# Kernel tuning notes

Hardware: AMD Instinct MI355X
Metric: run time of the kernel (lower is better)

The kernel has to match this reference:

```python
import jax, jax.numpy as jnp
import numpy as np


def _dct_basis_64() -> jnp.ndarray:
    """8x8 2D DCT-II basis as a conv filter of shape [8, 8, 1, 64] (HWIO).

    Filter k = 8*u + v is the (u, v) DCT basis function:
      alpha(u)*alpha(v)*cos((2x+1)u pi/16)*cos((2y+1)v pi/16)
    """
    N = 8
    xs = np.arange(N)
    # 1D DCT matrix: C[u, x]
    C = np.cos((2 * xs[None, :] + 1) * xs[:, None] * np.pi / (2 * N))
    alpha = np.full(N, np.sqrt(2.0 / N))
    alpha[0] = np.sqrt(1.0 / N)
    C = alpha[:, None] * C  # [u, x]
    # basis[x, y, u, v] = C[u, x] * C[v, y]
    basis = np.einsum('ux,vy->xyuv', C, C).reshape(N, N, 1, N * N)
    return jnp.asarray(basis, dtype=jnp.float32)


def setup_inputs() -> dict:
    key = jax.random.key(0)
    inputs = jax.random.normal(key, (16, 256, 256, 1), dtype=jnp.float32)
    dct_basis = _dct_basis_64()  # [8, 8, 1, 64]
    return {"inputs": inputs, "dct_basis": dct_basis}


def reference(inputs, dct_basis):
    # Block DCT: stride-8 SAME conv -> [B, 32, 32, 64]
    x = jax.lax.conv_general_dilated(
        inputs, dct_basis,
        window_strides=(8, 8), padding='SAME',
        dimension_numbers=('NHWC', 'HWIO', 'NHWC'))
    gamma = 1000000.0
    bins = jnp.arange(-60, 61, dtype=x.dtype)  # 121 thresholds
    # Soft CDF at every threshold in one vectorized pass:
    # [B, 121, Hc, Wc, 64] -> sum over spatial -> [B, 121, 64]
    s = jax.nn.sigmoid(gamma * (x[:, None] - bins[None, :, None, None, None]))
    x4 = jnp.sum(s, axis=(2, 3)) / 1024.0
    # Differentiate adjacent soft-CDF values -> 120-bin soft histogram
    x5 = x4[:, 0:120, :] - x4[:, 1:121, :]
    return x5[..., None]  # [B, 120, 64, 1]
```

## Files before the change

### kernel.cpp

```cpp
#include <hip/hip_runtime.h>
#include <math.h>


#define HSTRIDE 121

__global__ __launch_bounds__(64) void dct_hist_kernel(
    const float* __restrict__ in,
    const float* __restrict__ basis,
    float* __restrict__ out)
{
    __shared__ float hist[64 * HSTRIDE];

    const int t  = threadIdx.x;
    const int wg = blockIdx.x;
    const int b  = wg >> 4;
    const int q  = wg & 15;

    #pragma unroll
    for (int i = 0; i < HSTRIDE; ++i) hist[i * 64 + t] = 0.0f;
    __syncthreads();

    float Cm[8][8];
    #pragma unroll
    for (int a = 0; a < 8; ++a)
        #pragma unroll
        for (int x = 0; x < 8; ++x)
            Cm[a][x] = basis[x * 512 + a * 8] * 2.8284271247461903f;

    const int by = q * 2 + (t >> 5);
    const int bx = t & 31;
    const float* p0 = in + ((b * 256 + by * 8) * 256 + bx * 8);

    float tv[8][8];
    #pragma unroll
    for (int x = 0; x < 8; ++x) {
        const float4 r0 = *(const float4*)(p0 + x * 256);
        const float4 r1 = *(const float4*)(p0 + x * 256 + 4);
        const float p[8] = {r0.x, r0.y, r0.z, r0.w, r1.x, r1.y, r1.z, r1.w};
        #pragma unroll
        for (int v = 0; v < 8; ++v) {
            float s = 0.0f;
            #pragma unroll
            for (int y = 0; y < 8; ++y) s = fmaf(Cm[v][y], p[y], s);
            tv[x][v] = s;
        }
    }

    const float EPS = 3e-5f;
    #pragma unroll
    for (int u = 0; u < 8; ++u) {
        #pragma unroll
        for (int v = 0; v < 8; ++v) {
            float xv = 0.0f;
            #pragma unroll
            for (int x = 0; x < 8; ++x) xv = fmaf(Cm[u][x], tv[x][v], xv);
            const int k = u * 8 + v;

            const int j = (int)floorf(xv + 60.0f);
            if (j >= -1 && j <= 120) {
                const float bf  = (float)j - 60.0f;
                const float dlo = xv - bf;
                const float dhi = xv - (bf + 1.0f);
                if (dlo > EPS && dhi < -EPS) {
                    if (j >= 0 && j <= 119) atomicAdd(&hist[k * HSTRIDE + j], 1.0f);
                } else {
                    const float slo = 1.0f / (1.0f + expf(-1e6f * dlo));
                    const float shi = 1.0f / (1.0f + expf(-1e6f * dhi));
                    if (j >= 0 && j <= 119)     atomicAdd(&hist[k * HSTRIDE + j],     slo - shi);
                    if (j - 1 >= 0)             atomicAdd(&hist[k * HSTRIDE + j - 1], 1.0f - slo);
                    if (j + 1 <= 119)           atomicAdd(&hist[k * HSTRIDE + j + 1], shi);
                }
            }
        }
    }

    __syncthreads();

    float* outb = out + b * (120 * 64);
    for (int bin = 0; bin < 120; ++bin) {
        const float v = hist[t * HSTRIDE + bin];
        if (v != 0.0f) atomicAdd(&outb[bin * 64 + t], v * (1.0f / 1024.0f));
    }
}

extern "C" void kernel_launch(void* const* d_in, const int* in_sizes, int n_in,
                              void* d_out, int out_size, void* d_ws, size_t ws_size,
                              hipStream_t stream) {
    const float* inputs = (const float*)d_in[0];
    const float* basis  = (const float*)d_in[1];
    float* out = (float*)d_out;

    (void)hipMemsetAsync(out, 0, (size_t)out_size * sizeof(float), stream);

    dct_hist_kernel<<<dim3(256), dim3(64), 0, stream>>>(inputs, basis, out);
}
```

Before: 72.17 us.

## Use one 1024-thread workgroup per image with privatized LDS histograms

```diff
diff --git a/kernel.cpp b/kernel.cpp
--- a/kernel.cpp
+++ b/kernel.cpp
@@ -3,22 +3,19 @@
 
 
 #define HSTRIDE 121
+#define HCOPY   (64 * HSTRIDE)
 
-__global__ __launch_bounds__(64) void dct_hist_kernel(
+__global__ __launch_bounds__(1024) void dct_hist_kernel(
     const float* __restrict__ in,
     const float* __restrict__ basis,
     float* __restrict__ out)
 {
-    __shared__ float hist[64 * HSTRIDE];
+    __shared__ float hist[2 * HCOPY];
 
-    const int t  = threadIdx.x;
-    const int wg = blockIdx.x;
-    const int b  = wg >> 4;
-    const int q  = wg & 15;
+    const int t = threadIdx.x;
+    const int b = blockIdx.x;
 
-    #pragma unroll
-    for (int i = 0; i < HSTRIDE; ++i) hist[i * 64 + t] = 0.0f;
-    __syncthreads();
+    for (int i = t; i < 2 * HCOPY; i += 1024) hist[i] = 0.0f;
 
     float Cm[8][8];
     #pragma unroll
@@ -27,7 +24,9 @@
         for (int x = 0; x < 8; ++x)
             Cm[a][x] = basis[x * 512 + a * 8] * 2.8284271247461903f;
 
-    const int by = q * 2 + (t >> 5);
+    __syncthreads();
+
+    const int by = t >> 5;
     const int bx = t & 31;
     const float* p0 = in + ((b * 256 + by * 8) * 256 + bx * 8);
 
@@ -46,6 +45,7 @@
         }
     }
 
+    float* h = hist + ((t & 32) ? HCOPY : 0);
     const float EPS = 3e-5f;
     #pragma unroll
     for (int u = 0; u < 8; ++u) {
@@ -62,13 +62,13 @@
                 const float dlo = xv - bf;
                 const float dhi = xv - (bf + 1.0f);
                 if (dlo > EPS && dhi < -EPS) {
-                    if (j >= 0 && j <= 119) atomicAdd(&hist[k * HSTRIDE + j], 1.0f);
+                    if (j >= 0 && j <= 119) atomicAdd(&h[k * HSTRIDE + j], 1.0f);
                 } else {
                     const float slo = 1.0f / (1.0f + expf(-1e6f * dlo));
                     const float shi = 1.0f / (1.0f + expf(-1e6f * dhi));
-                    if (j >= 0 && j <= 119)     atomicAdd(&hist[k * HSTRIDE + j],     slo - shi);
-                    if (j - 1 >= 0)             atomicAdd(&hist[k * HSTRIDE + j - 1], 1.0f - slo);
-                    if (j + 1 <= 119)           atomicAdd(&hist[k * HSTRIDE + j + 1], shi);
+                    if (j >= 0 && j <= 119)     atomicAdd(&h[k * HSTRIDE + j],     slo - shi);
+                    if (j - 1 >= 0)             atomicAdd(&h[k * HSTRIDE + j - 1], 1.0f - slo);
+                    if (j + 1 <= 119)           atomicAdd(&h[k * HSTRIDE + j + 1], shi);
                 }
             }
         }
@@ -77,9 +77,11 @@
     __syncthreads();
 
     float* outb = out + b * (120 * 64);
-    for (int bin = 0; bin < 120; ++bin) {
-        const float v = hist[t * HSTRIDE + bin];
-        if (v != 0.0f) atomicAdd(&outb[bin * 64 + t], v * (1.0f / 1024.0f));
+    for (int idx = t; idx < 120 * 64; idx += 1024) {
+        const int bin = idx >> 6;
+        const int k   = idx & 63;
+        outb[idx] = (hist[k * HSTRIDE + bin] + hist[HCOPY + k * HSTRIDE + bin])
+                    * (1.0f / 1024.0f);
     }
 }
 
@@ -90,7 +92,5 @@
     const float* basis  = (const float*)d_in[1];
     float* out = (float*)d_out;
 
-    (void)hipMemsetAsync(out, 0, (size_t)out_size * sizeof(float), stream);
-
-    dct_hist_kernel<<<dim3(256), dim3(64), 0, stream>>>(inputs, basis, out);
+    dct_hist_kernel<<<dim3(16), dim3(1024), 0, stream>>>(inputs, basis, out);
 }
```

Measured after the change: 170.0 us. 136% more time.

## Split DCT across threads via shared memory and use register-packed histogram counters

Applied to the files above, without the earlier changes.

```diff
diff --git a/kernel.cpp b/kernel.cpp
--- a/kernel.cpp
+++ b/kernel.cpp
@@ -1,39 +1,38 @@
 #include <hip/hip_runtime.h>
 #include <math.h>
 
-
-#define HSTRIDE 121
 
 __global__ __launch_bounds__(64) void dct_hist_kernel(
     const float* __restrict__ in,
     const float* __restrict__ basis,
     float* __restrict__ out)
 {
-    __shared__ float hist[64 * HSTRIDE];
+    __shared__ float tvs[16 * 73];
+    __shared__ float coef[64 * 17];
 
     const int t  = threadIdx.x;
     const int wg = blockIdx.x;
-    const int b  = wg >> 4;
-    const int q  = wg & 15;
+    const int b  = wg >> 6;
+    const int g  = wg & 63;
+    const int by = g >> 1;
+    const int bx0 = (g & 1) * 16;
 
-    #pragma unroll
-    for (int i = 0; i < HSTRIDE; ++i) hist[i * 64 + t] = 0.0f;
-    __syncthreads();
+    const int i = t >> 2;
+    const int h = t & 3;
+
+    const float SQRT8 = 2.8284271247461903f;
 
     float Cm[8][8];
     #pragma unroll
     for (int a = 0; a < 8; ++a)
         #pragma unroll
         for (int x = 0; x < 8; ++x)
-            Cm[a][x] = basis[x * 512 + a * 8] * 2.8284271247461903f;
+            Cm[a][x] = basis[x * 512 + a * 8] * SQRT8;
 
-    const int by = q * 2 + (t >> 5);
-    const int bx = t & 31;
-    const float* p0 = in + ((b * 256 + by * 8) * 256 + bx * 8);
-
-    float tv[8][8];
+    const float* p0 = in + ((b * 256 + by * 8) * 256 + (bx0 + i) * 8);
     #pragma unroll
-    for (int x = 0; x < 8; ++x) {
+    for (int xl = 0; xl < 2; ++xl) {
+        const int x = 2 * h + xl;
         const float4 r0 = *(const float4*)(p0 + x * 256);
         const float4 r1 = *(const float4*)(p0 + x * 256 + 4);
         const float p[8] = {r0.x, r0.y, r0.z, r0.w, r1.x, r1.y, r1.z, r1.w};
@@ -42,44 +41,81 @@
             float s = 0.0f;
             #pragma unroll
             for (int y = 0; y < 8; ++y) s = fmaf(Cm[v][y], p[y], s);
-            tv[x][v] = s;
+            tvs[i * 73 + x * 9 + v] = s;
         }
     }
 
+    float Cu0[8], Cu1[8];
+    #pragma unroll
+    for (int x = 0; x < 8; ++x) {
+        Cu0[x] = basis[x * 512 + (2 * h) * 8] * SQRT8;
+        Cu1[x] = basis[x * 512 + (2 * h + 1) * 8] * SQRT8;
+    }
+
+    __syncthreads();
+
+    #pragma unroll
+    for (int v = 0; v < 8; ++v) {
+        float tcol[8];
+        #pragma unroll
+        for (int x = 0; x < 8; ++x) tcol[x] = tvs[i * 73 + x * 9 + v];
+        float xv0 = 0.0f, xv1 = 0.0f;
+        #pragma unroll
+        for (int x = 0; x < 8; ++x) {
+            xv0 = fmaf(Cu0[x], tcol[x], xv0);
+            xv1 = fmaf(Cu1[x], tcol[x], xv1);
+        }
+        coef[((2 * h) * 8 + v) * 17 + i] = xv0;
+        coef[((2 * h + 1) * 8 + v) * 17 + i] = xv1;
+    }
+
+    __syncthreads();
+
+    unsigned h0 = 0, h1 = 0, h2 = 0, h3 = 0, h4 = 0, h5 = 0;
+    float* outb = out + b * (120 * 64);
     const float EPS = 3e-5f;
+
     #pragma unroll
-    for (int u = 0; u < 8; ++u) {
-        #pragma unroll
-        for (int v = 0; v < 8; ++v) {
-            float xv = 0.0f;
-            #pragma unroll
-            for (int x = 0; x < 8; ++x) xv = fmaf(Cm[u][x], tv[x][v], xv);
-            const int k = u * 8 + v;
-
-            const int j = (int)floorf(xv + 60.0f);
-            if (j >= -1 && j <= 120) {
-                const float bf  = (float)j - 60.0f;
-                const float dlo = xv - bf;
-                const float dhi = xv - (bf + 1.0f);
-                if (dlo > EPS && dhi < -EPS) {
-                    if (j >= 0 && j <= 119) atomicAdd(&hist[k * HSTRIDE + j], 1.0f);
-                } else {
-                    const float slo = 1.0f / (1.0f + expf(-1e6f * dlo));
-                    const float shi = 1.0f / (1.0f + expf(-1e6f * dhi));
-                    if (j >= 0 && j <= 119)     atomicAdd(&hist[k * HSTRIDE + j],     slo - shi);
-                    if (j - 1 >= 0)             atomicAdd(&hist[k * HSTRIDE + j - 1], 1.0f - slo);
-                    if (j + 1 <= 119)           atomicAdd(&hist[k * HSTRIDE + j + 1], shi);
+    for (int blk = 0; blk < 16; ++blk) {
+        const float xv = coef[t * 17 + blk];
+        const int j = (int)floorf(xv + 60.0f);
+        if (j >= -1 && j <= 120) {
+            const float bf  = (float)j - 60.0f;
+            const float dlo = xv - bf;
+            const float dhi = xv - (bf + 1.0f);
+            if (dlo > EPS && dhi < -EPS) {
+                const unsigned w = (unsigned)(j - 48);
+                if (w < 24u) {
+                    const unsigned inc = 1u << (8 * (w & 3));
+                    const unsigned sel = w >> 2;
+                    h0 += (sel == 0) ? inc : 0u;
+                    h1 += (sel == 1) ? inc : 0u;
+                    h2 += (sel == 2) ? inc : 0u;
+                    h3 += (sel == 3) ? inc : 0u;
+                    h4 += (sel == 4) ? inc : 0u;
+                    h5 += (sel == 5) ? inc : 0u;
+                } else if (j >= 0 && j <= 119) {
+                    atomicAdd(&outb[j * 64 + t], 1.0f / 1024.0f);
                 }
+            } else {
+                const float slo = 1.0f / (1.0f + expf(-1e6f * dlo));
+                const float shi = 1.0f / (1.0f + expf(-1e6f * dhi));
+                if (j >= 0 && j <= 119)
+                    atomicAdd(&outb[j * 64 + t], (slo - shi) * (1.0f / 1024.0f));
+                if (j - 1 >= 0)
+                    atomicAdd(&outb[(j - 1) * 64 + t], (1.0f - slo) * (1.0f / 1024.0f));
+                if (j + 1 <= 119)
+                    atomicAdd(&outb[(j + 1) * 64 + t], shi * (1.0f / 1024.0f));
             }
         }
     }
 
-    __syncthreads();
-
-    float* outb = out + b * (120 * 64);
-    for (int bin = 0; bin < 120; ++bin) {
-        const float v = hist[t * HSTRIDE + bin];
-        if (v != 0.0f) atomicAdd(&outb[bin * 64 + t], v * (1.0f / 1024.0f));
+    const unsigned hw[6] = {h0, h1, h2, h3, h4, h5};
+    #pragma unroll
+    for (int w = 0; w < 24; ++w) {
+        const float cnt = (float)((hw[w >> 2] >> (8 * (w & 3))) & 255u);
+        if (cnt != 0.0f)
+            atomicAdd(&outb[(48 + w) * 64 + t], cnt * (1.0f / 1024.0f));
     }
 }
 
@@ -92,5 +128,5 @@
 
     (void)hipMemsetAsync(out, 0, (size_t)out_size * sizeof(float), stream);
 
-    dct_hist_kernel<<<dim3(256), dim3(64), 0, stream>>>(inputs, basis, out);
+    dct_hist_kernel<<<dim3(1024), dim3(64), 0, stream>>>(inputs, basis, out);
 }
```

After: 64.77 us. 1.11x faster.
